# Kernel optimization log

Measured on AMD Instinct MI355X. Metric: run time of the kernel, lower is better.

## Reference

```python
import jax, jax.numpy as jnp
import numpy as np

B, T, V, F, H, WIN = 512, 49, 34, 16, 64, 4
W = T - WIN + 1  # 46 sliding windows


def make_pe(max_len, d):
    pos = np.arange(max_len, dtype=np.float32)[:, None]
    div = np.exp(np.arange(0, d, 2, dtype=np.float32) * (-np.log(10000.0) / d))
    pe = np.zeros((max_len, d), dtype=np.float32)
    pe[:, 0::2] = np.sin(pos * div)
    pe[:, 1::2] = np.cos(pos * div)
    return jnp.asarray(pe)


def impute(arr, delta_ts, mask, w, b):
    # arr/mask [B,T,V], delta_ts [B,T]; serial masked cumulative-sum + LOCF scan
    missing = (mask == 0).astype(arr.dtype)
    dd = jnp.broadcast_to(delta_ts[:, :, None], arr.shape)

    def step(carry, inp):
        c_prev, x_prev = carry
        d_t, x_t, m_t = inp
        c_t = d_t + c_prev * m_t                      # cum delta resets at observations
        x_new = jnp.where(m_t > 0, x_prev, x_t)       # last-observation carry-forward
        return (c_t, x_new), (c_t, x_new)

    xs = (dd.swapaxes(0, 1)[1:], arr.swapaxes(0, 1)[1:], missing.swapaxes(0, 1)[1:])
    _, (c_rest, x_rest) = jax.lax.scan(step, (dd[:, 0], arr[:, 0]), xs)
    cum = jnp.concatenate([dd[:, :1], c_rest.swapaxes(0, 1)], axis=1)
    last = jnp.concatenate([arr[:, :1], x_rest.swapaxes(0, 1)], axis=1)
    cum = cum / jnp.max(cum)
    decay = jnp.exp(-jnp.clip(w * cum + b, 0.0, 1000.0))  # w,b broadcast [1,V]
    means = jnp.mean(arr, axis=1, keepdims=True)
    return arr * mask + (1 - mask) * (decay * last + (1 - decay) * means)


def gru_layer(x, Wih, Whh, bih, bhh):
    # torch GRU gate order r,z,n; Wih [in,3H], Whh [H,3H]
    nB = x.shape[0]
    Hh = Whh.shape[0]
    xW = x @ Wih + bih  # [B,T,3H] precomputed input projections

    def step(h, xw_t):
        gh = h @ Whh + bhh
        xr, xz, xn = jnp.split(xw_t, 3, axis=-1)
        hr, hz, hn = jnp.split(gh, 3, axis=-1)
        r = jax.nn.sigmoid(xr + hr)
        z = jax.nn.sigmoid(xz + hz)
        n = jnp.tanh(xn + r * hn)
        h_new = (1 - z) * n + z * h
        return h_new, h_new

    _, ys = jax.lax.scan(step, jnp.zeros((nB, Hh), x.dtype), xW.swapaxes(0, 1))
    return ys.swapaxes(0, 1)


def forward(arr, mask, time, w_input_decay, b_input_decay,
            enc_W1, enc_b1, enc_W2, enc_b2,
            tla_Wq, tla_bq, tla_Wk, tla_bk, tla_Wv, tla_bv,
            adj, mp_W1, mp_b1, mp_W2, mp_b2,
            sa_Wq, sa_bq, sa_Wk, sa_bk, sa_Wv, sa_bv,
            gru_Wih0, gru_Whh0, gru_bih0, gru_bhh0,
            gru_Wih1, gru_Whh1, gru_bih1, gru_bhh1,
            ta_Wq, ta_bq, ta_Wk, ta_bk, ta_Wv, ta_bv,
            cls_W1, cls_b1, cls_W2, cls_b2):
    tt = time.T  # [B,T]
    delta = jnp.concatenate([jnp.zeros((tt.shape[0], 1), tt.dtype), tt[:, 1:] - tt[:, :-1]], axis=1)
    x = impute(arr, delta, mask, w_input_decay, b_input_decay)  # [B,T,V]
    # per-variable 2-layer MLP encoders (batched over V via einsum)
    inp = jnp.stack([x, mask], axis=-1)  # [B,T,V,2]
    h = jax.nn.relu(jnp.einsum('btvi,vif->btvf', inp, enc_W1) + enc_b1)
    enc = jnp.einsum('btvf,vfg->btvg', h, enc_W2) + enc_b2  # [B,T,V,F]
    # sliding windows (torch unfold + permute) + window positional encoding
    idx = jnp.arange(W)[:, None] + jnp.arange(WIN)[None, :]
    win = enc[:, idx] + make_pe(WIN, F)[None, None, :, None, :]
    xw = win.reshape(B * W, WIN, V, F)
    # TimeLagAttentionLayer: separate attention per variable, batched via einsum
    q = jnp.einsum('blvf,vfg->blvg', xw, tla_Wq) + tla_bq
    k = jnp.einsum('blvf,vfg->blvg', xw, tla_Wk) + tla_bk
    v = jnp.einsum('blvf,vfg->blvg', xw, tla_Wv) + tla_bv
    scores = jnp.einsum('blvg,bmvg->bvlm', q, k) / jnp.sqrt(jnp.asarray(F, xw.dtype))
    att = jax.nn.softmax(scores, axis=-1)
    att_out = jnp.einsum('bvlm,bmvf->bvf', att, v)  # (att @ v) then sum over lag dim
    # MessagePassingLayer
    message = jnp.einsum('uv,bvf->buf', adj, att_out)
    mp_out = jax.nn.relu(message @ mp_W1 + mp_b1) @ mp_W2 + mp_b2  # [B*W,V,1] (t_out path)
    _ = mp_out
    latent = message
    l_out = latent.reshape(B, W, V, F).transpose(0, 2, 3, 1)  # [B,V,F,W]
    # SignalAttentionLayer (faithful: permute to [B,V,W,F] then raw reshape to [B*W,V,F])
    xs = l_out + make_pe(V, F)[None, :, :, None]
    xs = xs.transpose(0, 1, 3, 2).reshape(B * W, V, F)
    Q = xs @ sa_Wq + sa_bq
    K = xs @ sa_Wk + sa_bk
    Vv = xs @ sa_Wv + sa_bv
    sw = jax.nn.softmax(jnp.einsum('bnd,bmd->bnm', Q, K) / jnp.sqrt(jnp.asarray(F, xs.dtype)), axis=-1)
    s_out = jnp.einsum('bnm,bmd->bd', sw, Vv).reshape(B, W, F)  # (w @ V).sum(dim=1)
    # 2-layer GRU predictor
    g1 = gru_layer(s_out, gru_Wih0, gru_Whh0, gru_bih0, gru_bhh0)
    g2 = gru_layer(g1, gru_Wih1, gru_Whh1, gru_bih1, gru_bhh1)  # [B,W,H]
    # TemporalAttention pooling
    xt = g2 + make_pe(W, H)[None]
    Qt = xt @ ta_Wq + ta_bq
    Kt = xt @ ta_Wk + ta_bk
    Vt = xt @ ta_Wv + ta_bv
    tw = jax.nn.softmax(jnp.einsum('bld,bmd->blm', Qt, Kt) / jnp.sqrt(jnp.asarray(H, xt.dtype)), axis=-1)
    t_val = jnp.einsum('blm,bmd->bd', tw, Vt)  # [B,H]
    pred = jax.nn.relu(t_val @ cls_W1 + cls_b1) @ cls_W2 + cls_b2  # [B,1]
    return pred


def setup_inputs():
    key = jax.random.key(0)
    ks = jax.random.split(key, 48)

    def rn(k, shape, s=0.1):
        return jax.random.normal(k, shape, jnp.float32) * s

    d = {}
    d['arr'] = jax.random.normal(ks[0], (B, T, V), jnp.float32)
    d['mask'] = (jax.random.uniform(ks[1], (B, T, V)) < 0.7).astype(jnp.float32)
    d['time'] = jnp.cumsum(jax.random.uniform(ks[2], (T, B), jnp.float32), axis=0)
    d['w_input_decay'] = jnp.full((1, V), 0.1, jnp.float32)
    d['b_input_decay'] = jnp.zeros((1, V), jnp.float32)
    d['enc_W1'] = rn(ks[3], (V, 2, F), 0.5); d['enc_b1'] = rn(ks[4], (V, F))
    d['enc_W2'] = rn(ks[5], (V, F, F), 0.25); d['enc_b2'] = rn(ks[6], (V, F))
    d['tla_Wq'] = rn(ks[7], (V, F, F), 0.25); d['tla_bq'] = rn(ks[8], (V, F))
    d['tla_Wk'] = rn(ks[9], (V, F, F), 0.25); d['tla_bk'] = rn(ks[10], (V, F))
    d['tla_Wv'] = rn(ks[11], (V, F, F), 0.25); d['tla_bv'] = rn(ks[12], (V, F))
    d['adj'] = jnp.eye(V, dtype=jnp.float32) + 0.2 * jnp.ones((V, V), jnp.float32)
    d['mp_W1'] = rn(ks[13], (F, F), 0.25); d['mp_b1'] = rn(ks[14], (F,))
    d['mp_W2'] = rn(ks[15], (F, 1), 0.25); d['mp_b2'] = rn(ks[16], (1,))
    d['sa_Wq'] = rn(ks[17], (F, F), 0.25); d['sa_bq'] = rn(ks[18], (F,))
    d['sa_Wk'] = rn(ks[19], (F, F), 0.25); d['sa_bk'] = rn(ks[20], (F,))
    d['sa_Wv'] = rn(ks[21], (F, F), 0.25); d['sa_bv'] = rn(ks[22], (F,))
    d['gru_Wih0'] = rn(ks[23], (F, 3 * H), 0.2); d['gru_Whh0'] = rn(ks[24], (H, 3 * H), 0.1)
    d['gru_bih0'] = rn(ks[25], (3 * H,)); d['gru_bhh0'] = rn(ks[26], (3 * H,))
    d['gru_Wih1'] = rn(ks[27], (H, 3 * H), 0.1); d['gru_Whh1'] = rn(ks[28], (H, 3 * H), 0.1)
    d['gru_bih1'] = rn(ks[29], (3 * H,)); d['gru_bhh1'] = rn(ks[30], (3 * H,))
    d['ta_Wq'] = rn(ks[31], (H, H), 0.12); d['ta_bq'] = rn(ks[32], (H,))
    d['ta_Wk'] = rn(ks[33], (H, H), 0.12); d['ta_bk'] = rn(ks[34], (H,))
    d['ta_Wv'] = rn(ks[35], (H, H), 0.12); d['ta_bv'] = rn(ks[36], (H,))
    d['cls_W1'] = rn(ks[37], (H, H), 0.12); d['cls_b1'] = rn(ks[38], (H,))
    d['cls_W2'] = rn(ks[39], (H, 1), 0.12); d['cls_b2'] = rn(ks[40], (1,))
    return d


def reference(arr, mask, time, w_input_decay, b_input_decay,
              enc_W1, enc_b1, enc_W2, enc_b2,
              tla_Wq, tla_bq, tla_Wk, tla_bk, tla_Wv, tla_bv,
              adj, mp_W1, mp_b1, mp_W2, mp_b2,
              sa_Wq, sa_bq, sa_Wk, sa_bk, sa_Wv, sa_bv,
              gru_Wih0, gru_Whh0, gru_bih0, gru_bhh0,
              gru_Wih1, gru_Whh1, gru_bih1, gru_bhh1,
              ta_Wq, ta_bq, ta_Wk, ta_bk, ta_Wv, ta_bv,
              cls_W1, cls_b1, cls_W2, cls_b2):
    return forward(arr, mask, time, w_input_decay, b_input_decay,
                   enc_W1, enc_b1, enc_W2, enc_b2,
                   tla_Wq, tla_bq, tla_Wk, tla_bk, tla_Wv, tla_bv,
                   adj, mp_W1, mp_b1, mp_W2, mp_b2,
                   sa_Wq, sa_bq, sa_Wk, sa_bk, sa_Wv, sa_bv,
                   gru_Wih0, gru_Whh0, gru_bih0, gru_bhh0,
                   gru_Wih1, gru_Whh1, gru_bih1, gru_bhh1,
                   ta_Wq, ta_bq, ta_Wk, ta_bk, ta_Wv, ta_bv,
                   cls_W1, cls_b1, cls_W2, cls_b2)
```

## Files before the change

### kernel.cpp

```cpp
#include <hip/hip_runtime.h>
#include <math.h>

#define BB 512
#define TT 49
#define VV 34
#define FF 16
#define HH 64
#define WWIN 4
#define WW 46
#define BW (BB*WW)
#define TH3 (3*HH)
#define ROWS 25088
#define SG 2

#define SOUT_OFF   0ull
#define XW1_OFF    376832ull
#define G1_OFF     (XW1_OFF + 4521984ull)
#define XW2_OFF    (G1_OFF + 1507328ull)
#define G2_OFF     (XW2_OFF + 4521984ull)

#define MSG_SZ     12812288ull
#define CUM_SZ     852992ull
#define MEANS_SZ   17408ull
#define AO_OFF     12435456ull
#define MSG2_OFF   (AO_OFF + MSG_SZ)
#define CUM2_OFF   (MSG2_OFF + MSG_SZ)
#define LAST2_OFF  (CUM2_OFF + CUM_SZ)
#define MEANS2_OFF (LAST2_OFF + CUM_SZ)
#define MAX2_OFF   (MEANS2_OFF + MEANS_SZ)
#define PQ_OFF     (MAX2_OFF + 4ull)
#define SAW_OFF    (PQ_OFF + 6528ull)
#define FW_OFF     (SAW_OFF + 292ull)

__global__ __launch_bounds__(256) void k_scan(
    const float* __restrict__ arr, const float* __restrict__ msk,
    const float* __restrict__ timeTB,
    float* __restrict__ cum, float* __restrict__ last,
    float* __restrict__ means, unsigned int* __restrict__ maxv) {
  int tid = blockIdx.x * 256 + threadIdx.x;
  int b = tid / VV, v = tid - b * VV;
  const int base = b * TT * VV + v;
  float x = arr[base];
  float c = 0.f, lm = 0.f, s = x;
  cum[base] = 0.f;
  last[base] = x;
  float tp = timeTB[b];
  for (int t = 1; t < TT; ++t) {
    float tc = timeTB[t * BB + b];
    float d = tc - tp; tp = tc;
    int e = base + t * VV;
    float a = arr[e], m = msk[e];
    float miss = (m == 0.f) ? 1.f : 0.f;
    c = d + c * miss;
    x = (miss > 0.f) ? x : a;
    cum[e] = c; last[e] = x;
    lm = fmaxf(lm, c);
    s += a;
  }
  means[tid] = s * (1.f / 49.f);
  #pragma unroll
  for (int off = 32; off; off >>= 1) lm = fmaxf(lm, __shfl_xor(lm, off));
  if ((threadIdx.x & 63) == 0) atomicMax(maxv, __float_as_uint(lm));
}

__global__ __launch_bounds__(256) void k_prep(
    const float* __restrict__ tlaWq, const float* __restrict__ tlaWk,
    const float* __restrict__ tlaWv,
    const float* __restrict__ tlaBq, const float* __restrict__ tlaBk,
    const float* __restrict__ tlaBv,
    const float* __restrict__ saWq, const float* __restrict__ saBq,
    const float* __restrict__ saWk, const float* __restrict__ saBk,
    const float* __restrict__ encW2, const float* __restrict__ encB2,
    float* __restrict__ pqg, float* __restrict__ saw, float* __restrict__ fw) {
  const int bid = blockIdx.x;
  const int t = threadIdx.x;
  if (bid < 26) {
    int idx = bid * 256 + t;
    if (idx >= 6528) return;
    int which = idx / 2176;
    int r = idx - which * 2176;
    int l = r / 544;
    int rr = r - l * 544;
    int v = rr >> 4, f = rr & 15;
    const float* W = which == 0 ? tlaWq : which == 1 ? tlaWk : tlaWv;
    float acc = 0.f;
    #pragma unroll
    for (int i = 0; i < FF; ++i) {
      int i2 = i & ~1;
      float dv = expf(-logf(10000.f) * (float)i2 / (float)FF);
      float ang = (float)l * dv;
      float pe = (i & 1) ? cosf(ang) : sinf(ang);
      acc += pe * W[v * 256 + i * 16 + f];
    }
    pqg[idx] = acc;
  } else if (bid == 26) {
    int i = t & 15, j = t >> 4;
    float a = 0.f;
    #pragma unroll
    for (int f = 0; f < 16; ++f) a += saWq[i * 16 + f] * saWk[j * 16 + f];
    saw[j * 16 + i] = a;
    if (t < 16) {
      float pp = 0.f, qq = 0.f;
      #pragma unroll
      for (int f = 0; f < 16; ++f) { pp += saWq[t * 16 + f] * saBk[f]; qq += saWk[t * 16 + f] * saBq[f]; }
      saw[256 + t] = pp;
      saw[272 + t] = qq;
    }
    if (t == 0) {
      float c = 0.f;
      #pragma unroll
      for (int f = 0; f < 16; ++f) c += saBq[f] * saBk[f];
      saw[288] = c;
    }
  } else {
    const int v = bid - 27;
    const int f = t >> 4, o = t & 15;
    const float* W2v = encW2 + v * 256;
    float cq = 0.f, ck = 0.f, cv = 0.f;
    #pragma unroll
    for (int g = 0; g < 16; ++g) {
      float w2 = W2v[f * 16 + g];
      cq += w2 * tlaWq[v * 256 + g * 16 + o];
      ck += w2 * tlaWk[v * 256 + g * 16 + o];
      cv += w2 * tlaWv[v * 256 + g * 16 + o];
    }
    fw[v * 816 + 0 * 272 + f * 16 + o] = cq;
    fw[v * 816 + 1 * 272 + f * 16 + o] = ck;
    fw[v * 816 + 2 * 272 + f * 16 + o] = cv;
    if (t < 48) {
      int which = t >> 4, o2 = t & 15;
      const float* Wp = which == 0 ? tlaWq : which == 1 ? tlaWk : tlaWv;
      const float* Bp = which == 0 ? tlaBq : which == 1 ? tlaBk : tlaBv;
      float acc = Bp[v * 16 + o2];
      #pragma unroll
      for (int g = 0; g < 16; ++g) acc += encB2[v * 16 + g] * Wp[v * 256 + g * 16 + o2];
      fw[v * 816 + which * 272 + 256 + o2] = acc;
    }
  }
}

__global__ __launch_bounds__(256) void k_enc4(
    const float* __restrict__ arr, const float* __restrict__ msk,
    const float* __restrict__ cum, const float* __restrict__ last,
    const float* __restrict__ means, const unsigned int* __restrict__ maxv,
    const float* __restrict__ wdec, const float* __restrict__ bdec,
    const float* __restrict__ W1, const float* __restrict__ B1,
    const float* __restrict__ fw, const float* __restrict__ pqg,
    float* __restrict__ ao) {
  __shared__ float pkv[4][3][TT * 17];
  const int v = blockIdx.x % VV;
  const int bgrp = blockIdx.x / VV;
  const int tid = threadIdx.x;
  const int wave = tid >> 6, lane = tid & 63;
  const int b = bgrp * 4 + wave;
  const float* fv = fw + v * 816;
  if (lane < TT) {
    const int t = lane;
    const int idx = (b * TT + t) * VV + v;
    float inv = 1.f / __uint_as_float(*maxv);
    float a = arr[idx], m = msk[idx];
    float cc = cum[idx] * inv;
    float ttc = fminf(fmaxf(wdec[v] * cc + bdec[v], 0.f), 1000.f);
    float dec = expf(-ttc);
    float xx = a * m + (1.f - m) * (dec * last[idx] + (1.f - dec) * means[b * VV + v]);
    float h[16];
    #pragma unroll
    for (int f = 0; f < 16; ++f)
      h[f] = fmaxf(xx * W1[v * 32 + f] + m * W1[v * 32 + 16 + f] + B1[v * 16 + f], 0.f);
    #pragma unroll
    for (int which = 0; which < 3; ++which) {
      const float* C = fv + which * 272;
      #pragma unroll
      for (int g = 0; g < 16; ++g) {
        float acc = C[256 + g];
        #pragma unroll
        for (int f = 0; f < 16; ++f) acc += h[f] * C[f * 16 + g];
        pkv[wave][which][t * 17 + g] = acc;
      }
    }
  }
  __syncthreads();
  if (lane < WW) {
    const int w = lane;
    const float* P = &pkv[wave][0][0];
    const float* K = &pkv[wave][1][0];
    const float* Vp = &pkv[wave][2][0];
    float kk[4][16];
    #pragma unroll
    for (int m = 0; m < 4; ++m)
      #pragma unroll
      for (int f = 0; f < 16; ++f)
        kk[m][f] = K[(w + m) * 17 + f] + pqg[2176 + m * 544 + v * 16 + f];
    float sc[4][4];
    #pragma unroll
    for (int l = 0; l < 4; ++l) {
      float qv[16];
      #pragma unroll
      for (int i = 0; i < 16; ++i)
        qv[i] = P[(w + l) * 17 + i] + pqg[l * 544 + v * 16 + i];
      #pragma unroll
      for (int m = 0; m < 4; ++m) {
        float s = 0.f;
        #pragma unroll
        for (int i = 0; i < 16; ++i) s += qv[i] * kk[m][i];
        sc[l][m] = s * 0.25f;
      }
    }
    float csum[4] = {0.f, 0.f, 0.f, 0.f};
    #pragma unroll
    for (int l = 0; l < 4; ++l) {
      float mx = fmaxf(fmaxf(sc[l][0], sc[l][1]), fmaxf(sc[l][2], sc[l][3]));
      float sum = 0.f;
      #pragma unroll
      for (int m = 0; m < 4; ++m) { sc[l][m] = expf(sc[l][m] - mx); sum += sc[l][m]; }
      float r = 1.f / sum;
      #pragma unroll
      for (int m = 0; m < 4; ++m) csum[m] += sc[l][m] * r;
    }
    float outv[16];
    #pragma unroll
    for (int f = 0; f < 16; ++f) outv[f] = 0.f;
    #pragma unroll
    for (int m = 0; m < 4; ++m) {
      float c = csum[m];
      #pragma unroll
      for (int f = 0; f < 16; ++f)
        outv[f] += c * (Vp[(w + m) * 17 + f] + pqg[2 * 2176 + m * 544 + v * 16 + f]);
    }
    float4* d4 = (float4*)(ao + ((size_t)(b * VV + v) * WW + w) * 16);
    #pragma unroll
    for (int j = 0; j < 4; ++j)
      d4[j] = make_float4(outv[4*j], outv[4*j+1], outv[4*j+2], outv[4*j+3]);
  }
}

#define MPW 12
__global__ __launch_bounds__(256) void k_mp(
    const float* __restrict__ ao, const float* __restrict__ adj,
    float* __restrict__ msg2) {
  __shared__ float adjs[VV * VV];
  __shared__ __align__(16) float aos[VV][MPW * 16];
  __shared__ float pes[VV * 16];
  const int bb = blockIdx.x >> 2;
  const int wt = blockIdx.x & 3;
  const int w0 = wt * MPW;
  const int wc = (wt == 3) ? (WW - 3 * MPW) : MPW;
  const int tid = threadIdx.x;
  for (int i = tid; i < VV * VV; i += 256) adjs[i] = adj[i];
  for (int i = tid; i < VV * 16; i += 256) {
    int u = i >> 4, f = i & 15;
    int f2 = f & ~1;
    float dv = expf(-logf(10000.f) * (float)f2 / 16.f);
    float ang = (float)u * dv;
    pes[i] = (f & 1) ? cosf(ang) : sinf(ang);
  }
  const int nq = wc * 4;
  for (int i = tid; i < VV * nq; i += 256) {
    int vv2 = i / nq, r = i - vv2 * nq;
    int wl = r >> 2, q = r & 3;
    float4 val = *(const float4*)(ao + ((size_t)(bb * VV + vv2) * WW + w0 + wl) * 16 + q * 4);
    *(float4*)&aos[vv2][wl * 16 + q * 4] = val;
  }
  __syncthreads();
  for (int i = tid; i < VV * nq; i += 256) {
    int u = i / nq, r = i - u * nq;
    int wl = r >> 2, q = r & 3;
    float a0 = 0.f, a1 = 0.f, a2 = 0.f, a3 = 0.f;
    for (int vv2 = 0; vv2 < VV; ++vv2) {
      float a = adjs[u * VV + vv2];
      float4 s = *(const float4*)&aos[vv2][wl * 16 + q * 4];
      a0 += a * s.x; a1 += a * s.y; a2 += a * s.z; a3 += a * s.w;
    }
    float4 o = make_float4(a0 + pes[u * 16 + q * 4],
                           a1 + pes[u * 16 + q * 4 + 1],
                           a2 + pes[u * 16 + q * 4 + 2],
                           a3 + pes[u * 16 + q * 4 + 3]);
    *(float4*)(msg2 + ((size_t)(bb * VV + u) * WW + w0 + wl) * 16 + q * 4) = o;
  }
}

__global__ __launch_bounds__(256) void k_sa3(
    const float* __restrict__ msg2, const float* __restrict__ saw,
    const float* __restrict__ Wv, const float* __restrict__ bv,
    float* __restrict__ sout) {
  __shared__ float As[256];
  __shared__ float ps[16], q2s[16];
  __shared__ float xs[SG][VV][20];
  __shared__ float zs[SG][VV][17];
  __shared__ float sc[SG][VV][35];
  __shared__ float uws[SG][VV], vws[SG][VV];
  __shared__ float rs[SG][VV], cs[SG][VV];
  __shared__ float ys[SG][16];
  __shared__ float c0s;
  const int tid = threadIdx.x;
  const int n0 = blockIdx.x * SG;
  As[tid] = saw[tid];
  if (tid < 16) { ps[tid] = saw[256 + tid]; q2s[tid] = saw[272 + tid]; }
  if (tid == 0) c0s = saw[288];
  {
    const float4* src = (const float4*)(msg2 + (size_t)n0 * (VV * FF));
    for (int i = tid; i < SG * VV * 4; i += 256) {
      int g = i / 136, r = i - g * 136;
      int m = r >> 2, i4 = r & 3;
      float4 val = src[i];
      float* d = &xs[g][m][i4 * 4];
      d[0] = val.x; d[1] = val.y; d[2] = val.z; d[3] = val.w;
    }
  }
  __syncthreads();
  for (int idx = tid; idx < SG * VV * FF; idx += 256) {
    int g = idx / 544, r = idx - g * 544;
    int m = r >> 4, i = r & 15;
    float acc = 0.f;
    #pragma unroll
    for (int j = 0; j < FF; ++j) acc += As[j * 16 + i] * xs[g][m][j];
    zs[g][m][i] = acc;
  }
  if (tid < SG * VV) {
    int g = tid / VV, m = tid - g * VV;
    float pu = 0.f, pv = 0.f;
    #pragma unroll
    for (int i = 0; i < FF; ++i) { float x = xs[g][m][i]; pu += x * ps[i]; pv += x * q2s[i]; }
    uws[g][m] = pu; vws[g][m] = pv;
  }
  __syncthreads();
  for (int idx = tid; idx < SG * 17 * 17; idx += 256) {
    int g = idx / 289, r = idx - g * 289;
    int lt = r / 17, mt = r - lt * 17;
    int l0 = lt * 2, m0 = mt * 2;
    float s00 = 0.f, s01 = 0.f, s10 = 0.f, s11 = 0.f;
    #pragma unroll
    for (int i = 0; i < FF; ++i) {
      float x0 = xs[g][l0][i], x1 = xs[g][l0 + 1][i];
      float z0 = zs[g][m0][i], z1 = zs[g][m0 + 1][i];
      s00 += x0 * z0; s01 += x0 * z1; s10 += x1 * z0; s11 += x1 * z1;
    }
    float c0 = c0s;
    float ul0 = uws[g][l0], ul1 = uws[g][l0 + 1];
    float vm0 = vws[g][m0], vm1 = vws[g][m0 + 1];
    sc[g][l0][m0]         = (s00 + ul0 + vm0 + c0) * 0.25f;
    sc[g][l0][m0 + 1]     = (s01 + ul0 + vm1 + c0) * 0.25f;
    sc[g][l0 + 1][m0]     = (s10 + ul1 + vm0 + c0) * 0.25f;
    sc[g][l0 + 1][m0 + 1] = (s11 + ul1 + vm1 + c0) * 0.25f;
  }
  __syncthreads();
  if (tid < SG * VV) {
    int g = tid / VV, l = tid - g * VV;
    float mx = -1e30f;
    for (int m = 0; m < VV; ++m) mx = fmaxf(mx, sc[g][l][m]);
    float sum = 0.f;
    for (int m = 0; m < VV; ++m) { float e = expf(sc[g][l][m] - mx); sc[g][l][m] = e; sum += e; }
    rs[g][l] = 1.f / sum;
  }
  __syncthreads();
  if (tid < SG * VV) {
    int g = tid / VV, m = tid - g * VV;
    float acc = 0.f;
    for (int l = 0; l < VV; ++l) acc += sc[g][l][m] * rs[g][l];
    cs[g][m] = acc;
  }
  __syncthreads();
  if (tid < SG * FF) {
    int g = tid >> 4, i = tid & 15;
    float acc = 0.f;
    for (int m = 0; m < VV; ++m) acc += cs[g][m] * xs[g][m][i];
    ys[g][i] = acc;
  }
  __syncthreads();
  if (tid < SG * FF) {
    int g = tid >> 4, f = tid & 15;
    float acc = 34.f * bv[f];
    #pragma unroll
    for (int i = 0; i < FF; ++i) acc += ys[g][i] * Wv[i * 16 + f];
    sout[(size_t)(n0 + g) * FF + f] = acc;
  }
}

__global__ __launch_bounds__(256) void k_xw1(
    const float* __restrict__ x, const float* __restrict__ Wih,
    const float* __restrict__ bih, float* __restrict__ xw) {
  int t = blockIdx.x * 256 + threadIdx.x;
  int n = t / TH3, o = t - n * TH3;
  float acc = bih[o];
  const float* xr = x + (size_t)n * FF;
  #pragma unroll
  for (int i = 0; i < FF; ++i) acc += xr[i] * Wih[i * TH3 + o];
  xw[t] = acc;
}

__global__ __launch_bounds__(192) void k_xw2(
    const float* __restrict__ x, const float* __restrict__ Wih,
    const float* __restrict__ bih, float* __restrict__ xw) {
  __shared__ float xsh[16][HH];
  int n0 = blockIdx.x * 16;
  int tid = threadIdx.x;
  for (int idx = tid; idx < 16 * HH; idx += 192) {
    int ns = idx >> 6, i = idx & 63;
    xsh[ns][i] = x[(size_t)(n0 + ns) * HH + i];
  }
  __syncthreads();
  float acc[16];
  float bb = bih[tid];
  #pragma unroll
  for (int ns = 0; ns < 16; ++ns) acc[ns] = bb;
  for (int i = 0; i < HH; ++i) {
    float wv = Wih[i * TH3 + tid];
    #pragma unroll
    for (int ns = 0; ns < 16; ++ns) acc[ns] += xsh[ns][i] * wv;
  }
  #pragma unroll
  for (int ns = 0; ns < 16; ++ns) xw[(size_t)(n0 + ns) * TH3 + tid] = acc[ns];
}

__global__ __launch_bounds__(192) void k_gru(
    const float* __restrict__ xw, const float* __restrict__ Whh,
    const float* __restrict__ bhh, float* __restrict__ gout) {
  __shared__ float whh[HH * TH3];
  __shared__ float hsh[HH];
  __shared__ float gh[TH3];
  int tid = threadIdx.x;
  int b = blockIdx.x;
  for (int i = tid; i < HH * TH3; i += 192) whh[i] = Whh[i];
  if (tid < HH) hsh[tid] = 0.f;
  float bb = bhh[tid];
  __syncthreads();
  for (int w = 0; w < WW; ++w) {
    float acc = bb;
    #pragma unroll 8
    for (int i = 0; i < HH; ++i) acc += hsh[i] * whh[i * TH3 + tid];
    gh[tid] = acc;
    __syncthreads();
    if (tid < HH) {
      const float* xr = xw + (size_t)(b * WW + w) * TH3;
      float r = 1.f / (1.f + expf(-(xr[tid] + gh[tid])));
      float z = 1.f / (1.f + expf(-(xr[HH + tid] + gh[HH + tid])));
      float nn = tanhf(xr[2 * HH + tid] + r * gh[2 * HH + tid]);
      float hn = (1.f - z) * nn + z * hsh[tid];
      hsh[tid] = hn;
      gout[(size_t)(b * WW + w) * HH + tid] = hn;
    }
    __syncthreads();
  }
}

__global__ __launch_bounds__(256) void k_ta(
    const float* __restrict__ g2,
    const float* __restrict__ Wq, const float* __restrict__ bq,
    const float* __restrict__ Wk, const float* __restrict__ bk,
    const float* __restrict__ Wv, const float* __restrict__ bv,
    const float* __restrict__ cW1, const float* __restrict__ cb1,
    const float* __restrict__ cW2, const float* __restrict__ cb2,
    float* __restrict__ out) {
  __shared__ float xt[WW * 65];
  __shared__ float QKVs[3][WW * 65];
  __shared__ float sc[WW * WW];
  __shared__ float cs[WW];
  __shared__ float tval[HH];
  __shared__ float hrelu[HH];
  int tid = threadIdx.x;
  int b = blockIdx.x;
  for (int idx = tid; idx < WW * HH; idx += 256) {
    int w = idx >> 6, d = idx & 63;
    int f2 = d & ~1;
    float dv = expf(-logf(10000.f) * (float)f2 / (float)HH);
    float ang = (float)w * dv;
    float pe = (d & 1) ? cosf(ang) : sinf(ang);
    xt[w * 65 + d] = g2[(size_t)(b * WW + w) * HH + d] + pe;
  }
  __syncthreads();
  if (tid < 192) {
    int which = tid >> 6, d = tid & 63;
    const float* Wt = which == 0 ? Wq : which == 1 ? Wk : Wv;
    float bias = (which == 0 ? bq : which == 1 ? bk : bv)[d];
    float col[HH];
    #pragma unroll
    for (int i = 0; i < HH; ++i) col[i] = Wt[i * HH + d];
    float* dst = &QKVs[which][0];
    for (int w = 0; w < WW; ++w) {
      float acc = bias;
      #pragma unroll
      for (int i = 0; i < HH; ++i) acc += xt[w * 65 + i] * col[i];
      dst[w * 65 + d] = acc;
    }
  }
  __syncthreads();
  for (int idx = tid; idx < WW * WW; idx += 256) {
    int l = idx / WW, m = idx - l * WW;
    float s = 0.f;
    #pragma unroll
    for (int i = 0; i < HH; ++i) s += QKVs[0][l * 65 + i] * QKVs[1][m * 65 + i];
    sc[idx] = s * 0.125f;
  }
  __syncthreads();
  if (tid < WW) {
    float mx = -1e30f;
    for (int m = 0; m < WW; ++m) mx = fmaxf(mx, sc[tid * WW + m]);
    float sum = 0.f;
    for (int m = 0; m < WW; ++m) { float e = expf(sc[tid * WW + m] - mx); sc[tid * WW + m] = e; sum += e; }
    float r = 1.f / sum;
    for (int m = 0; m < WW; ++m) sc[tid * WW + m] *= r;
  }
  __syncthreads();
  if (tid < WW) {
    float s = 0.f;
    for (int l = 0; l < WW; ++l) s += sc[l * WW + tid];
    cs[tid] = s;
  }
  __syncthreads();
  if (tid < HH) {
    float acc = 0.f;
    for (int m = 0; m < WW; ++m) acc += cs[m] * QKVs[2][m * 65 + tid];
    tval[tid] = acc;
  }
  __syncthreads();
  if (tid < HH) {
    float acc = cb1[tid];
    #pragma unroll
    for (int d = 0; d < HH; ++d) acc += tval[d] * cW1[d * HH + tid];
    hrelu[tid] = fmaxf(acc, 0.f);
  }
  __syncthreads();
  if (tid == 0) {
    float acc = cb2[0];
    for (int j = 0; j < HH; ++j) acc += hrelu[j] * cW2[j];
    out[b] = acc;
  }
}

extern "C" void kernel_launch(void* const* d_in, const int* in_sizes, int n_in,
                              void* d_out, int out_size, void* d_ws, size_t ws_size,
                              hipStream_t stream) {
  (void)in_sizes; (void)n_in; (void)out_size; (void)ws_size;
  const float* arr    = (const float*)d_in[0];
  const float* msk    = (const float*)d_in[1];
  const float* timeTB = (const float*)d_in[2];
  const float* wdec   = (const float*)d_in[3];
  const float* bdec   = (const float*)d_in[4];
  const float* encW1  = (const float*)d_in[5];
  const float* encB1  = (const float*)d_in[6];
  const float* encW2  = (const float*)d_in[7];
  const float* encB2  = (const float*)d_in[8];
  const float* tlaWq  = (const float*)d_in[9];
  const float* tlaBq  = (const float*)d_in[10];
  const float* tlaWk  = (const float*)d_in[11];
  const float* tlaBk  = (const float*)d_in[12];
  const float* tlaWv  = (const float*)d_in[13];
  const float* tlaBv  = (const float*)d_in[14];
  const float* adj    = (const float*)d_in[15];
  const float* saWq   = (const float*)d_in[20];
  const float* saBq   = (const float*)d_in[21];
  const float* saWk   = (const float*)d_in[22];
  const float* saBk   = (const float*)d_in[23];
  const float* saWv   = (const float*)d_in[24];
  const float* saBv   = (const float*)d_in[25];
  const float* gWih0  = (const float*)d_in[26];
  const float* gWhh0  = (const float*)d_in[27];
  const float* gBih0  = (const float*)d_in[28];
  const float* gBhh0  = (const float*)d_in[29];
  const float* gWih1  = (const float*)d_in[30];
  const float* gWhh1  = (const float*)d_in[31];
  const float* gBih1  = (const float*)d_in[32];
  const float* gBhh1  = (const float*)d_in[33];
  const float* taWq   = (const float*)d_in[34];
  const float* taBq   = (const float*)d_in[35];
  const float* taWk   = (const float*)d_in[36];
  const float* taBk   = (const float*)d_in[37];
  const float* taWv   = (const float*)d_in[38];
  const float* taBv   = (const float*)d_in[39];
  const float* cW1    = (const float*)d_in[40];
  const float* cb1    = (const float*)d_in[41];
  const float* cW2    = (const float*)d_in[42];
  const float* cb2    = (const float*)d_in[43];
  float* out = (float*)d_out;
  float* ws  = (float*)d_ws;

  float* ao    = ws + AO_OFF;
  float* msg2  = ws + MSG2_OFF;
  float* cum   = ws + CUM2_OFF;
  float* last  = ws + LAST2_OFF;
  float* means = ws + MEANS2_OFF;
  unsigned int* maxv = (unsigned int*)(ws + MAX2_OFF);
  float* pqg   = ws + PQ_OFF;
  float* saw   = ws + SAW_OFF;
  float* fw    = ws + FW_OFF;

  float* sout = ws + SOUT_OFF;
  float* xw1  = ws + XW1_OFF;
  float* g1   = ws + G1_OFF;
  float* xw2  = ws + XW2_OFF;
  float* g2   = ws + G2_OFF;

  hipMemsetAsync(maxv, 0, sizeof(unsigned int), stream);
  k_scan<<<68, 256, 0, stream>>>(arr, msk, timeTB, cum, last, means, maxv);
  k_prep<<<61, 256, 0, stream>>>(tlaWq, tlaWk, tlaWv, tlaBq, tlaBk, tlaBv,
                                 saWq, saBq, saWk, saBk, encW2, encB2,
                                 pqg, saw, fw);
  k_enc4<<<VV * 128, 256, 0, stream>>>(arr, msk, cum, last, means, maxv,
                                       wdec, bdec, encW1, encB1, fw, pqg, ao);
  k_mp<<<BB * 4, 256, 0, stream>>>(ao, adj, msg2);
  k_sa3<<<BW / SG, 256, 0, stream>>>(msg2, saw, saWv, saBv, sout);
  k_xw1<<<(BW * TH3) / 256, 256, 0, stream>>>(sout, gWih0, gBih0, xw1);
  k_gru<<<BB, 192, 0, stream>>>(xw1, gWhh0, gBhh0, g1);
  k_xw2<<<BW / 16, 192, 0, stream>>>(g1, gWih1, gBih1, xw2);
  k_gru<<<BB, 192, 0, stream>>>(xw2, gWhh1, gBhh1, g2);
  k_ta<<<BB, 256, 0, stream>>>(g2, taWq, taBq, taWk, taBk, taWv, taBv,
                               cW1, cb1, cW2, cb2, out);
}
```

Measured before the change: 408.0 us.

## Fold value projection into GRU input weights, register-resident single-wave GRU

Precomputes the product of the spatial-attention value weights with the first GRU input weights, plus a combined bias, in the prep kernel. The attention kernel then writes the GRU layer-0 input projections directly, which removes the separate k_xw1 kernel and the sout round trip. The score computation is retiled to 4x4 register blocks with float4 shared-memory reads. The GRU is rewritten as a single 64-thread wave that keeps Whh in registers and broadcasts h with readlane, removing shared-memory traffic and block barriers per step, at the cost of heavy register pressure (192 weight registers per thread).

```diff
diff --git a/kernel.cpp b/kernel.cpp
--- a/kernel.cpp
+++ b/kernel.cpp
@@ -6,7 +6,6 @@
 #define VV 34
 #define FF 16
 #define HH 64
-#define WWIN 4
 #define WW 46
 #define BW (BB*WW)
 #define TH3 (3*HH)
@@ -31,6 +30,8 @@
 #define PQ_OFF     (MAX2_OFF + 4ull)
 #define SAW_OFF    (PQ_OFF + 6528ull)
 #define FW_OFF     (SAW_OFF + 292ull)
+#define WVIH_OFF   (FW_OFF + 27744ull)
+#define BIAS2_OFF  (WVIH_OFF + 3072ull)
 
 __global__ __launch_bounds__(256) void k_scan(
     const float* __restrict__ arr, const float* __restrict__ msk,
@@ -70,8 +71,11 @@
     const float* __restrict__ tlaBv,
     const float* __restrict__ saWq, const float* __restrict__ saBq,
     const float* __restrict__ saWk, const float* __restrict__ saBk,
+    const float* __restrict__ saWv, const float* __restrict__ saBv,
     const float* __restrict__ encW2, const float* __restrict__ encB2,
-    float* __restrict__ pqg, float* __restrict__ saw, float* __restrict__ fw) {
+    const float* __restrict__ Wih0, const float* __restrict__ bih0,
+    float* __restrict__ pqg, float* __restrict__ saw, float* __restrict__ fw,
+    float* __restrict__ wvih, float* __restrict__ bias2) {
   const int bid = blockIdx.x;
   const int t = threadIdx.x;
   if (bid < 26) {
@@ -112,7 +116,7 @@
       for (int f = 0; f < 16; ++f) c += saBq[f] * saBk[f];
       saw[288] = c;
     }
-  } else {
+  } else if (bid < 61) {
     const int v = bid - 27;
     const int f = t >> 4, o = t & 15;
     const float* W2v = encW2 + v * 256;
@@ -135,6 +139,20 @@
       #pragma unroll
       for (int g = 0; g < 16; ++g) acc += encB2[v * 16 + g] * Wp[v * 256 + g * 16 + o2];
       fw[v * 816 + which * 272 + 256 + o2] = acc;
+    }
+  } else if (bid < 73) {
+    int idx = (bid - 61) * 256 + t;
+    int i = idx / 192, o = idx - i * 192;
+    float acc = 0.f;
+    #pragma unroll
+    for (int f = 0; f < 16; ++f) acc += saWv[i * 16 + f] * Wih0[f * 192 + o];
+    wvih[idx] = acc;
+  } else {
+    if (t < 192) {
+      float acc = bih0[t];
+      #pragma unroll
+      for (int f = 0; f < 16; ++f) acc += 34.f * saBv[f] * Wih0[f * 192 + t];
+      bias2[t] = acc;
     }
   }
 }
@@ -279,17 +297,18 @@
   }
 }
 
-__global__ __launch_bounds__(256) void k_sa3(
+#define DOT4(a,b) ((a).x*(b).x + (a).y*(b).y + (a).z*(b).z + (a).w*(b).w)
+__global__ __launch_bounds__(256) void k_sa4(
     const float* __restrict__ msg2, const float* __restrict__ saw,
-    const float* __restrict__ Wv, const float* __restrict__ bv,
-    float* __restrict__ sout) {
+    const float* __restrict__ wvih, const float* __restrict__ bias2,
+    float* __restrict__ xw1) {
   __shared__ float As[256];
   __shared__ float ps[16], q2s[16];
-  __shared__ float xs[SG][VV][20];
-  __shared__ float zs[SG][VV][17];
-  __shared__ float sc[SG][VV][35];
-  __shared__ float uws[SG][VV], vws[SG][VV];
-  __shared__ float rs[SG][VV], cs[SG][VV];
+  __shared__ __align__(16) float xs[SG][36][20];
+  __shared__ __align__(16) float zs[SG][36][20];
+  __shared__ float sc[SG][36][37];
+  __shared__ float uws[SG][36], vws[SG][36];
+  __shared__ float rs[SG][34], cs[SG][34];
   __shared__ float ys[SG][16];
   __shared__ float c0s;
   const int tid = threadIdx.x;
@@ -298,94 +317,147 @@
   if (tid < 16) { ps[tid] = saw[256 + tid]; q2s[tid] = saw[272 + tid]; }
   if (tid == 0) c0s = saw[288];
   {
-    const float4* src = (const float4*)(msg2 + (size_t)n0 * (VV * FF));
-    for (int i = tid; i < SG * VV * 4; i += 256) {
+    const float4* src = (const float4*)(msg2 + (size_t)n0 * 544);
+    for (int i = tid; i < SG * 136; i += 256) {
       int g = i / 136, r = i - g * 136;
-      int m = r >> 2, i4 = r & 3;
-      float4 val = src[i];
-      float* d = &xs[g][m][i4 * 4];
-      d[0] = val.x; d[1] = val.y; d[2] = val.z; d[3] = val.w;
-    }
-  }
-  __syncthreads();
-  for (int idx = tid; idx < SG * VV * FF; idx += 256) {
-    int g = idx / 544, r = idx - g * 544;
-    int m = r >> 4, i = r & 15;
+      int m = r >> 2, q = r & 3;
+      ((float4*)&xs[g][m][0])[q] = src[i];
+    }
+  }
+  __syncthreads();
+  for (int idx = tid; idx < SG * 136; idx += 256) {
+    int g = idx / 136, r = idx - g * 136;
+    int m0 = (r >> 3) * 2, i0 = (r & 7) * 2;
+    float z00 = 0.f, z01 = 0.f, z10 = 0.f, z11 = 0.f;
+    #pragma unroll
+    for (int jc = 0; jc < 4; ++jc) {
+      float4 xa = ((const float4*)&xs[g][m0][0])[jc];
+      float4 xb = ((const float4*)&xs[g][m0 + 1][0])[jc];
+      #pragma unroll
+      for (int jj = 0; jj < 4; ++jj) {
+        int j = jc * 4 + jj;
+        float xj0 = (jj == 0) ? xa.x : (jj == 1) ? xa.y : (jj == 2) ? xa.z : xa.w;
+        float xj1 = (jj == 0) ? xb.x : (jj == 1) ? xb.y : (jj == 2) ? xb.z : xb.w;
+        float a0 = As[j * 16 + i0], a1 = As[j * 16 + i0 + 1];
+        z00 += a0 * xj0; z01 += a1 * xj0; z10 += a0 * xj1; z11 += a1 * xj1;
+      }
+    }
+    zs[g][m0][i0] = z00; zs[g][m0][i0 + 1] = z01;
+    zs[g][m0 + 1][i0] = z10; zs[g][m0 + 1][i0 + 1] = z11;
+  }
+  if (tid < SG * 34) {
+    int g = tid / 34, m = tid - g * 34;
+    float pu = 0.f, pv = 0.f;
+    #pragma unroll
+    for (int i = 0; i < 16; ++i) { float x = xs[g][m][i]; pu += x * ps[i]; pv += x * q2s[i]; }
+    uws[g][m] = pu; vws[g][m] = pv;
+  }
+  __syncthreads();
+  for (int idx = tid; idx < SG * 81; idx += 256) {
+    int g = idx / 81, r = idx - g * 81;
+    int l0 = (r / 9) * 4, m0 = (r - (r / 9) * 9) * 4;
+    float s00=0,s01=0,s02=0,s03=0, s10=0,s11=0,s12=0,s13=0;
+    float s20=0,s21=0,s22=0,s23=0, s30=0,s31=0,s32=0,s33=0;
+    #pragma unroll
+    for (int ic = 0; ic < 4; ++ic) {
+      float4 x0 = ((const float4*)&xs[g][l0 + 0][0])[ic];
+      float4 x1 = ((const float4*)&xs[g][l0 + 1][0])[ic];
+      float4 x2 = ((const float4*)&xs[g][l0 + 2][0])[ic];
+      float4 x3 = ((const float4*)&xs[g][l0 + 3][0])[ic];
+      float4 z0 = ((const float4*)&zs[g][m0 + 0][0])[ic];
+      float4 z1 = ((const float4*)&zs[g][m0 + 1][0])[ic];
+      float4 z2 = ((const float4*)&zs[g][m0 + 2][0])[ic];
+      float4 z3 = ((const float4*)&zs[g][m0 + 3][0])[ic];
+      s00 += DOT4(x0,z0); s01 += DOT4(x0,z1); s02 += DOT4(x0,z2); s03 += DOT4(x0,z3);
+      s10 += DOT4(x1,z0); s11 += DOT4(x1,z1); s12 += DOT4(x1,z2); s13 += DOT4(x1,z3);
+      s20 += DOT4(x2,z0); s21 += DOT4(x2,z1); s22 += DOT4(x2,z2); s23 += DOT4(x2,z3);
+      s30 += DOT4(x3,z0); s31 += DOT4(x3,z1); s32 += DOT4(x3,z2); s33 += DOT4(x3,z3);
+    }
+    float c0 = c0s;
+    float u0 = uws[g][l0], u1 = uws[g][l0+1], u2 = uws[g][l0+2], u3 = uws[g][l0+3];
+    float v0 = vws[g][m0], v1 = vws[g][m0+1], v2 = vws[g][m0+2], v3 = vws[g][m0+3];
+    sc[g][l0+0][m0+0] = (s00+u0+v0+c0)*0.25f; sc[g][l0+0][m0+1] = (s01+u0+v1+c0)*0.25f;
+    sc[g][l0+0][m0+2] = (s02+u0+v2+c0)*0.25f; sc[g][l0+0][m0+3] = (s03+u0+v3+c0)*0.25f;
+    sc[g][l0+1][m0+0] = (s10+u1+v0+c0)*0.25f; sc[g][l0+1][m0+1] = (s11+u1+v1+c0)*0.25f;
+    sc[g][l0+1][m0+2] = (s12+u1+v2+c0)*0.25f; sc[g][l0+1][m0+3] = (s13+u1+v3+c0)*0.25f;
+    sc[g][l0+2][m0+0] = (s20+u2+v0+c0)*0.25f; sc[g][l0+2][m0+1] = (s21+u2+v1+c0)*0.25f;
+    sc[g][l0+2][m0+2] = (s22+u2+v2+c0)*0.25f; sc[g][l0+2][m0+3] = (s23+u2+v3+c0)*0.25f;
+    sc[g][l0+3][m0+0] = (s30+u3+v0+c0)*0.25f; sc[g][l0+3][m0+1] = (s31+u3+v1+c0)*0.25f;
+    sc[g][l0+3][m0+2] = (s32+u3+v2+c0)*0.25f; sc[g][l0+3][m0+3] = (s33+u3+v3+c0)*0.25f;
+  }
+  __syncthreads();
+  if (tid < SG * 34) {
+    int g = tid / 34, l = tid - g * 34;
+    float mx = -1e30f;
+    for (int m = 0; m < 34; ++m) mx = fmaxf(mx, sc[g][l][m]);
+    float sum = 0.f;
+    for (int m = 0; m < 34; ++m) { float e = expf(sc[g][l][m] - mx); sc[g][l][m] = e; sum += e; }
+    rs[g][l] = 1.f / sum;
+  }
+  __syncthreads();
+  if (tid < SG * 34) {
+    int g = tid / 34, m = tid - g * 34;
     float acc = 0.f;
-    #pragma unroll
-    for (int j = 0; j < FF; ++j) acc += As[j * 16 + i] * xs[g][m][j];
-    zs[g][m][i] = acc;
-  }
-  if (tid < SG * VV) {
-    int g = tid / VV, m = tid - g * VV;
-    float pu = 0.f, pv = 0.f;
-    #pragma unroll
-    for (int i = 0; i < FF; ++i) { float x = xs[g][m][i]; pu += x * ps[i]; pv += x * q2s[i]; }
-    uws[g][m] = pu; vws[g][m] = pv;
-  }
-  __syncthreads();
-  for (int idx = tid; idx < SG * 17 * 17; idx += 256) {
-    int g = idx / 289, r = idx - g * 289;
-    int lt = r / 17, mt = r - lt * 17;
-    int l0 = lt * 2, m0 = mt * 2;
-    float s00 = 0.f, s01 = 0.f, s10 = 0.f, s11 = 0.f;
-    #pragma unroll
-    for (int i = 0; i < FF; ++i) {
-      float x0 = xs[g][l0][i], x1 = xs[g][l0 + 1][i];
-      float z0 = zs[g][m0][i], z1 = zs[g][m0 + 1][i];
-      s00 += x0 * z0; s01 += x0 * z1; s10 += x1 * z0; s11 += x1 * z1;
-    }
-    float c0 = c0s;
-    float ul0 = uws[g][l0], ul1 = uws[g][l0 + 1];
-    float vm0 = vws[g][m0], vm1 = vws[g][m0 + 1];
-    sc[g][l0][m0]         = (s00 + ul0 + vm0 + c0) * 0.25f;
-    sc[g][l0][m0 + 1]     = (s01 + ul0 + vm1 + c0) * 0.25f;
-    sc[g][l0 + 1][m0]     = (s10 + ul1 + vm0 + c0) * 0.25f;
-    sc[g][l0 + 1][m0 + 1] = (s11 + ul1 + vm1 + c0) * 0.25f;
-  }
-  __syncthreads();
-  if (tid < SG * VV) {
-    int g = tid / VV, l = tid - g * VV;
-    float mx = -1e30f;
-    for (int m = 0; m < VV; ++m) mx = fmaxf(mx, sc[g][l][m]);
-    float sum = 0.f;
-    for (int m = 0; m < VV; ++m) { float e = expf(sc[g][l][m] - mx); sc[g][l][m] = e; sum += e; }
-    rs[g][l] = 1.f / sum;
-  }
-  __syncthreads();
-  if (tid < SG * VV) {
-    int g = tid / VV, m = tid - g * VV;
-    float acc = 0.f;
-    for (int l = 0; l < VV; ++l) acc += sc[g][l][m] * rs[g][l];
+    for (int l = 0; l < 34; ++l) acc += sc[g][l][m] * rs[g][l];
     cs[g][m] = acc;
   }
   __syncthreads();
-  if (tid < SG * FF) {
+  if (tid < SG * 16) {
     int g = tid >> 4, i = tid & 15;
     float acc = 0.f;
-    for (int m = 0; m < VV; ++m) acc += cs[g][m] * xs[g][m][i];
+    for (int m = 0; m < 34; ++m) acc += cs[g][m] * xs[g][m][i];
     ys[g][i] = acc;
   }
   __syncthreads();
-  if (tid < SG * FF) {
-    int g = tid >> 4, f = tid & 15;
-    float acc = 34.f * bv[f];
-    #pragma unroll
-    for (int i = 0; i < FF; ++i) acc += ys[g][i] * Wv[i * 16 + f];
-    sout[(size_t)(n0 + g) * FF + f] = acc;
-  }
-}
-
-__global__ __launch_bounds__(256) void k_xw1(
-    const float* __restrict__ x, const float* __restrict__ Wih,
-    const float* __restrict__ bih, float* __restrict__ xw) {
-  int t = blockIdx.x * 256 + threadIdx.x;
-  int n = t / TH3, o = t - n * TH3;
-  float acc = bih[o];
-  const float* xr = x + (size_t)n * FF;
+  for (int idx = tid; idx < SG * 192; idx += 256) {
+    int g = idx / 192, o = idx - g * 192;
+    float acc = bias2[o];
+    #pragma unroll
+    for (int i = 0; i < 16; ++i) acc += ys[g][i] * wvih[i * 192 + o];
+    xw1[(size_t)(n0 + g) * 192 + o] = acc;
+  }
+}
+
+#define RL(x,i) __uint_as_float(__builtin_amdgcn_readlane(__float_as_uint(x), (i)))
+__global__ __launch_bounds__(64) void k_gru2(
+    const float* __restrict__ xw, const float* __restrict__ Whh,
+    const float* __restrict__ bhh, float* __restrict__ gout) {
+  const int tid = threadIdx.x;
+  const int b = blockIdx.x;
+  float wr[64], wz[64], wn[64];
   #pragma unroll
-  for (int i = 0; i < FF; ++i) acc += xr[i] * Wih[i * TH3 + o];
-  xw[t] = acc;
+  for (int i = 0; i < 64; ++i) {
+    wr[i] = Whh[i * 192 + tid];
+    wz[i] = Whh[i * 192 + 64 + tid];
+    wn[i] = Whh[i * 192 + 128 + tid];
+  }
+  const float br = bhh[tid], bz = bhh[64 + tid], bn = bhh[128 + tid];
+  float h = 0.f;
+  const float* xr = xw + (size_t)b * WW * 192;
+  for (int w = 0; w < WW; ++w, xr += 192) {
+    float xrv = xr[tid], xzv = xr[64 + tid], xnv = xr[128 + tid];
+    float pr0 = br, pr1 = 0.f, pr2 = 0.f, pr3 = 0.f;
+    float pz0 = bz, pz1 = 0.f, pz2 = 0.f, pz3 = 0.f;
+    float pn0 = bn, pn1 = 0.f, pn2 = 0.f, pn3 = 0.f;
+    #pragma unroll
+    for (int i = 0; i < 64; i += 4) {
+      float h0 = RL(h, i), h1 = RL(h, i + 1), h2 = RL(h, i + 2), h3 = RL(h, i + 3);
+      pr0 += h0 * wr[i];     pr1 += h1 * wr[i + 1];
+      pr2 += h2 * wr[i + 2]; pr3 += h3 * wr[i + 3];
+      pz0 += h0 * wz[i];     pz1 += h1 * wz[i + 1];
+      pz2 += h2 * wz[i + 2]; pz3 += h3 * wz[i + 3];
+      pn0 += h0 * wn[i];     pn1 += h1 * wn[i + 1];
+      pn2 += h2 * wn[i + 2]; pn3 += h3 * wn[i + 3];
+    }
+    float ar = (pr0 + pr1) + (pr2 + pr3);
+    float az = (pz0 + pz1) + (pz2 + pz3);
+    float an = (pn0 + pn1) + (pn2 + pn3);
+    float r = 1.f / (1.f + expf(-(xrv + ar)));
+    float z = 1.f / (1.f + expf(-(xzv + az)));
+    float n = tanhf(xnv + r * an);
+    h = (1.f - z) * n + z * h;
+    gout[((size_t)b * WW + w) * HH + tid] = h;
+  }
 }
 
 __global__ __launch_bounds__(192) void k_xw2(
@@ -410,37 +482,6 @@
   }
   #pragma unroll
   for (int ns = 0; ns < 16; ++ns) xw[(size_t)(n0 + ns) * TH3 + tid] = acc[ns];
-}
-
-__global__ __launch_bounds__(192) void k_gru(
-    const float* __restrict__ xw, const float* __restrict__ Whh,
-    const float* __restrict__ bhh, float* __restrict__ gout) {
-  __shared__ float whh[HH * TH3];
-  __shared__ float hsh[HH];
-  __shared__ float gh[TH3];
-  int tid = threadIdx.x;
-  int b = blockIdx.x;
-  for (int i = tid; i < HH * TH3; i += 192) whh[i] = Whh[i];
-  if (tid < HH) hsh[tid] = 0.f;
-  float bb = bhh[tid];
-  __syncthreads();
-  for (int w = 0; w < WW; ++w) {
-    float acc = bb;
-    #pragma unroll 8
-    for (int i = 0; i < HH; ++i) acc += hsh[i] * whh[i * TH3 + tid];
-    gh[tid] = acc;
-    __syncthreads();
-    if (tid < HH) {
-      const float* xr = xw + (size_t)(b * WW + w) * TH3;
-      float r = 1.f / (1.f + expf(-(xr[tid] + gh[tid])));
-      float z = 1.f / (1.f + expf(-(xr[HH + tid] + gh[HH + tid])));
-      float nn = tanhf(xr[2 * HH + tid] + r * gh[2 * HH + tid]);
-      float hn = (1.f - z) * nn + z * hsh[tid];
-      hsh[tid] = hn;
-      gout[(size_t)(b * WW + w) * HH + tid] = hn;
-    }
-    __syncthreads();
-  }
 }
 
 __global__ __launch_bounds__(256) void k_ta(
@@ -583,8 +624,9 @@
   float* pqg   = ws + PQ_OFF;
   float* saw   = ws + SAW_OFF;
   float* fw    = ws + FW_OFF;
-
-  float* sout = ws + SOUT_OFF;
+  float* wvih  = ws + WVIH_OFF;
+  float* bias2 = ws + BIAS2_OFF;
+
   float* xw1  = ws + XW1_OFF;
   float* g1   = ws + G1_OFF;
   float* xw2  = ws + XW2_OFF;
@@ -592,17 +634,17 @@
 
   hipMemsetAsync(maxv, 0, sizeof(unsigned int), stream);
   k_scan<<<68, 256, 0, stream>>>(arr, msk, timeTB, cum, last, means, maxv);
-  k_prep<<<61, 256, 0, stream>>>(tlaWq, tlaWk, tlaWv, tlaBq, tlaBk, tlaBv,
-                                 saWq, saBq, saWk, saBk, encW2, encB2,
-                                 pqg, saw, fw);
+  k_prep<<<74, 256, 0, stream>>>(tlaWq, tlaWk, tlaWv, tlaBq, tlaBk, tlaBv,
+                                 saWq, saBq, saWk, saBk, saWv, saBv,
+                                 encW2, encB2, gWih0, gBih0,
+                                 pqg, saw, fw, wvih, bias2);
   k_enc4<<<VV * 128, 256, 0, stream>>>(arr, msk, cum, last, means, maxv,
                                        wdec, bdec, encW1, encB1, fw, pqg, ao);
   k_mp<<<BB * 4, 256, 0, stream>>>(ao, adj, msg2);
-  k_sa3<<<BW / SG, 256, 0, stream>>>(msg2, saw, saWv, saBv, sout);
-  k_xw1<<<(BW * TH3) / 256, 256, 0, stream>>>(sout, gWih0, gBih0, xw1);
-  k_gru<<<BB, 192, 0, stream>>>(xw1, gWhh0, gBhh0, g1);
+  k_sa4<<<BW / SG, 256, 0, stream>>>(msg2, saw, wvih, bias2, xw1);
+  k_gru2<<<BB, 64, 0, stream>>>(xw1, gWhh0, gBhh0, g1);
   k_xw2<<<BW / 16, 192, 0, stream>>>(g1, gWih1, gBih1, xw2);
-  k_gru<<<BB, 192, 0, stream>>>(xw2, gWhh1, gBhh1, g2);
+  k_gru2<<<BB, 64, 0, stream>>>(xw2, gWhh1, gBhh1, g2);
   k_ta<<<BB, 256, 0, stream>>>(g2, taWq, taBq, taWk, taBk, taWv, taBv,
                                cW1, cb1, cW2, cb2, out);
 }
```

After: 347.1 us. 14.9% less time.
